# Kernel optimization log

Measured on AMD Instinct MI355X. Metric: run time of the kernel, lower is better.

## Reference

```python
import jax, jax.numpy as jnp
import numpy as np

BN_EPS = 1e-5


def conv(x, w, b=None, stride=1, pad=1):
    out = jax.lax.conv_general_dilated(
        x, w, (stride, stride), [(pad, pad), (pad, pad)],
        dimension_numbers=("NCHW", "OIHW", "NCHW"))
    if b is not None:
        out = out + b[None, :, None, None]
    return out


def bn_relu(x):
    # BatchNorm2d(affine=False) in training mode: per-channel batch stats
    mean = jnp.mean(x, axis=(0, 2, 3), keepdims=True)
    var = jnp.var(x, axis=(0, 2, 3), keepdims=True)
    return jax.nn.relu((x - mean) * jax.lax.rsqrt(var + BN_EPS))


def deform_conv(x, offset, w, b, stride, pad=1):
    # torchvision DeformConv2d semantics, 3x3 kernel, dilation=1
    B, C, H, W = x.shape
    O = w.shape[0]
    K = 9
    Ho, Wo = offset.shape[2], offset.shape[3]
    off = offset.reshape(B, K, 2, Ho, Wo)  # (dy, dx) per kernel tap
    ky, kx = jnp.meshgrid(jnp.arange(3), jnp.arange(3), indexing="ij")
    ky = ky.reshape(K).astype(x.dtype)
    kx = kx.reshape(K).astype(x.dtype)
    oy = (jnp.arange(Ho) * stride - pad).astype(x.dtype)
    ox = (jnp.arange(Wo) * stride - pad).astype(x.dtype)
    # sampling coords [B,K,Ho,Wo]
    ys = oy[None, None, :, None] + ky[None, :, None, None] + off[:, :, 0]
    xs = ox[None, None, None, :] + kx[None, :, None, None] + off[:, :, 1]
    y0 = jnp.floor(ys)
    x0 = jnp.floor(xs)
    wy1 = ys - y0
    wx1 = xs - x0
    imf = x.reshape(B, C, H * W)

    def gather(iy, ix):
        valid = (iy >= 0) & (iy <= H - 1) & (ix >= 0) & (ix <= W - 1)
        iyc = jnp.clip(iy, 0, H - 1).astype(jnp.int32)
        ixc = jnp.clip(ix, 0, W - 1).astype(jnp.int32)
        lin = iyc * W + ixc  # [B,K,Ho,Wo]
        g = jax.vmap(lambda im, li: im[:, li])(imf, lin)  # [B,C,K,Ho,Wo]
        return g * valid[:, None].astype(x.dtype)

    sampled = (gather(y0, x0) * ((1 - wy1) * (1 - wx1))[:, None]
               + gather(y0, x0 + 1) * ((1 - wy1) * wx1)[:, None]
               + gather(y0 + 1, x0) * (wy1 * (1 - wx1))[:, None]
               + gather(y0 + 1, x0 + 1) * (wy1 * wx1)[:, None])
    out = jnp.einsum("ock,bckhw->bohw", w.reshape(O, C, K), sampled)
    return out + b[None, :, None, None]


def avgpool4(x):
    B, C, H, W = x.shape
    return x.reshape(B, C, H // 4, 4, W // 4, 4).mean(axis=(3, 5))


def setup_inputs() -> dict:
    key = jax.random.key(0)
    ks = jax.random.split(key, 20)
    n = jax.random.normal
    s = 0.05
    return {
        "x": n(ks[0], (8, 3, 640, 640), jnp.float32),
        "w_off1": n(ks[1], (18, 3, 3, 3), jnp.float32) * s,
        "b_off1": jnp.zeros((18,), jnp.float32),
        "w_d1": n(ks[2], (64, 3, 3, 3), jnp.float32) * s,
        "b_d1": jnp.zeros((64,), jnp.float32),
        "w_skip": n(ks[3], (64, 3, 1, 1), jnp.float32) * s,
        "b_skip": jnp.zeros((64,), jnp.float32),
        "w_bl1": n(ks[4], (64, 64, 3, 3), jnp.float32) * s,
        "w_bl2": n(ks[5], (64, 64, 3, 3), jnp.float32) * s,
        "w_off2": n(ks[6], (18, 64, 3, 3), jnp.float32) * s,
        "b_off2": jnp.zeros((18,), jnp.float32),
        "w_d2": n(ks[7], (64, 64, 3, 3), jnp.float32) * s,
        "b_d2": jnp.zeros((64,), jnp.float32),
        "w_off3": n(ks[8], (18, 64, 3, 3), jnp.float32) * s,
        "b_off3": jnp.zeros((18,), jnp.float32),
        "w_d3": n(ks[9], (256, 64, 3, 3), jnp.float32) * s,
        "b_d3": jnp.zeros((256,), jnp.float32),
    }


def reference(x, w_off1, b_off1, w_d1, b_d1, w_skip, b_skip, w_bl1, w_bl2,
              w_off2, b_off2, w_d2, b_d2, w_off3, b_off3, w_d3, b_d3):
    offset1 = conv(x, w_off1, b_off1, stride=4)
    d1 = deform_conv(x, offset1, w_d1, b_d1, stride=4)
    skip = conv(avgpool4(x), w_skip, b_skip, stride=1, pad=0)
    f = bn_relu(conv(d1 + skip, w_bl1))
    feat_1_4 = bn_relu(conv(f, w_bl2))
    offset2 = conv(feat_1_4, w_off2, b_off2, stride=2)
    feat_1_8 = deform_conv(feat_1_4, offset2, w_d2, b_d2, stride=2)
    offset3 = conv(feat_1_8, w_off3, b_off3, stride=2)
    feat_1_16 = deform_conv(feat_1_8, offset3, w_d3, b_d3, stride=2)
    return (feat_1_4, feat_1_8, feat_1_16)
```

## Files before the change

kernel.cpp:

```cpp
#include <hip/hip_runtime.h>
#include <hip/hip_bf16.h>
#include <math.h>

#define TPB 256

typedef __attribute__((ext_vector_type(8))) short bf16x8_t;
typedef __attribute__((ext_vector_type(4))) float f32x4_t;
typedef __attribute__((ext_vector_type(4))) int i32x4_t;
typedef __attribute__((ext_vector_type(4))) unsigned short u16x4_t;

static __device__ __forceinline__ float bf16_to_f(unsigned short s) {
    union { unsigned u; float f; } cv;
    cv.u = ((unsigned)s) << 16;
    return cv.f;
}
static __device__ __forceinline__ short f_to_bf16(float v) {
    __hip_bfloat16 h = __float2bfloat16(v);
    return *(short*)&h;
}

__global__ void repack_frag_kernel(const float* __restrict__ w,
                                   short* __restrict__ wtf,
                                   int Oreal, int NFRAG)
{
    int idx = blockIdx.x * TPB + threadIdx.x;
    int total = 18 * NFRAG * 64 * 8;
    if (idx >= total) return;
    int j    = idx & 7;
    int lane = (idx >> 3) & 63;
    int t    = idx >> 9;
    int ocf  = t % NFRAG;
    int kc   = t / NFRAG;
    int oc   = ocf * 16 + (lane & 15);
    int tap  = kc >> 1;
    int ic   = (kc & 1) * 32 + (lane >> 4) * 8 + j;
    float v = 0.f;
    if (oc < Oreal)
        v = w[((size_t)(oc * 64 + ic)) * 9 + tap];
    wtf[idx] = f_to_bf16(v);
}

__global__ __launch_bounds__(256, 1) void conv3x3_mfma_kernel(
    const short* __restrict__ xh,
    const short* __restrict__ wt,
    short* __restrict__ outh,
    float* __restrict__ stats)
{
    __shared__ short tile[18 * 18 * 64];
    __shared__ float sstat[128];
    const int H = 160, W = 160, HW = 25600;
    int blk = blockIdx.x;
    int b  = blk / 100;
    int r  = blk % 100;
    int y0 = (r / 10) * 16;
    int x0 = (r % 10) * 16;
    const int tid = threadIdx.x;

    const short* inb = xh + (size_t)b * HW * 64;
    for (int item = tid; item < 18 * 18 * 8; item += TPB) {
        int c8  = item & 7;
        int pix = item >> 3;
        int col = pix % 18, row = pix / 18;
        int y = y0 + row - 1;
        int x = x0 + col - 1;
        bf16x8_t v = {};
        if (y >= 0 && y < H && x >= 0 && x < W)
            v = *(const bf16x8_t*)&inb[((size_t)y * W + x) * 64 + c8 * 8];
        int ch = c8 ^ (col & 7);
        *(bf16x8_t*)&tile[(row * 18 + col) * 64 + ch * 8] = v;
    }
    if (tid < 128) sstat[tid] = 0.f;
    __syncthreads();

    const int wv  = tid >> 6;
    const int l   = tid & 63;
    const int l15 = l & 15;
    const int lg  = l >> 4;

    f32x4_t acc[4][4];
#pragma unroll
    for (int i = 0; i < 4; ++i)
#pragma unroll
        for (int j = 0; j < 4; ++j)
            acc[i][j] = (f32x4_t){0.f, 0.f, 0.f, 0.f};

    bf16x8_t bfp[2][4], afp[2][4];
#pragma unroll
    for (int nf = 0; nf < 4; ++nf)
        bfp[0][nf] = *(const bf16x8_t*)(wt + (((size_t)(0 * 4 + nf)) * 64 + l) * 8);
    {
        int colr = l15;
        int chunk = lg ^ (colr & 7);
#pragma unroll
        for (int mf = 0; mf < 4; ++mf)
            afp[0][mf] = *(const bf16x8_t*)&tile[((wv * 4 + mf) * 18 + colr) * 64 + chunk * 8];
    }
#pragma unroll
    for (int kc = 0; kc < 18; ++kc) {
        const int cur = kc & 1, nxt = cur ^ 1;
        if (kc + 1 < 18) {
            int kn = kc + 1;
#pragma unroll
            for (int nf = 0; nf < 4; ++nf)
                bfp[nxt][nf] = *(const bf16x8_t*)(wt + (((size_t)(kn * 4 + nf)) * 64 + l) * 8);
            int tap = kn >> 1;
            int dy = tap / 3, dx = tap % 3;
            int colr = l15 + dx;
            int chunk = (((kn & 1) << 2) + lg) ^ (colr & 7);
#pragma unroll
            for (int mf = 0; mf < 4; ++mf)
                afp[nxt][mf] = *(const bf16x8_t*)&tile[((wv * 4 + mf + dy) * 18 + colr) * 64 + chunk * 8];
        }
#pragma unroll
        for (int mf = 0; mf < 4; ++mf)
#pragma unroll
            for (int nf = 0; nf < 4; ++nf)
                acc[mf][nf] = __builtin_amdgcn_mfma_f32_16x16x32_bf16(
                    afp[cur][mf], bfp[cur][nf], acc[mf][nf], 0, 0, 0);
    }

    short* outb = outh + (size_t)b * HW * 64;
#pragma unroll
    for (int mf = 0; mf < 4; ++mf) {
        int y = y0 + wv * 4 + mf;
#pragma unroll
        for (int nf = 0; nf < 4; ++nf) {
            int oc = nf * 16 + l15;
#pragma unroll
            for (int k = 0; k < 4; ++k)
                outb[((size_t)y * W + x0 + lg * 4 + k) * 64 + oc] = f_to_bf16(acc[mf][nf][k]);
        }
    }

#pragma unroll
    for (int nf = 0; nf < 4; ++nf) {
        float s = 0.f, s2 = 0.f;
#pragma unroll
        for (int mf = 0; mf < 4; ++mf)
#pragma unroll
            for (int k = 0; k < 4; ++k) {
                float v = acc[mf][nf][k];
                s += v; s2 += v * v;
            }
        s  += __shfl_xor(s, 16, 64);  s  += __shfl_xor(s, 32, 64);
        s2 += __shfl_xor(s2, 16, 64); s2 += __shfl_xor(s2, 32, 64);
        if (lg == 0) {
            int oc = nf * 16 + l15;
            atomicAdd(&sstat[oc], s);
            atomicAdd(&sstat[64 + oc], s2);
        }
    }
    __syncthreads();
    float* st = stats + (size_t)(blockIdx.x & 7) * 128;
    if (tid < 128) atomicAdd(&st[tid], sstat[tid]);
}

__global__ void nchw_to_nhwc_bf16_kernel(const float* __restrict__ in,
                                         short* __restrict__ out, int HW)
{
    __shared__ short tile[64][66];
    int nchunks = HW >> 6;
    int b  = blockIdx.x / nchunks;
    int p0 = (blockIdx.x % nchunks) << 6;
    int tid = threadIdx.x;
#pragma unroll
    for (int rep = 0; rep < 16; ++rep) {
        int item = rep * 256 + tid;
        int c = item >> 6, p = item & 63;
        tile[p][c] = f_to_bf16(in[((size_t)b * 64 + c) * HW + p0 + p]);
    }
    __syncthreads();
#pragma unroll
    for (int rep = 0; rep < 16; ++rep) {
        int item = rep * 256 + tid;
        int p = item >> 6, c = item & 63;
        out[((size_t)b * HW + p0 + p) * 64 + c] = tile[p][c];
    }
}

__global__ void bn_apply_elem_kernel(const short* __restrict__ in,
                                     const float* __restrict__ stats,
                                     short* __restrict__ outh,
                                     float invN)
{
    __shared__ float sm[64], sr[64];
    int tid = threadIdx.x;
    if (tid < 64) {
        float s = 0.f, s2 = 0.f;
#pragma unroll
        for (int k = 0; k < 8; ++k) {
            s  += stats[k * 128 + tid];
            s2 += stats[k * 128 + 64 + tid];
        }
        float mean = s * invN;
        float var  = s2 * invN - mean * mean;
        sm[tid] = mean;
        sr[tid] = rsqrtf(var + 1e-5f);
    }
    __syncthreads();
    int item = blockIdx.x * TPB + tid;
    int c0 = (item & 7) * 8;
    bf16x8_t v = *(const bf16x8_t*)&in[(size_t)item * 8];
    bf16x8_t o;
#pragma unroll
    for (int j = 0; j < 8; ++j) {
        float f = (bf16_to_f((unsigned short)v[j]) - sm[c0 + j]) * sr[c0 + j];
        o[j] = f_to_bf16(f > 0.f ? f : 0.f);
    }
    *(bf16x8_t*)&outh[(size_t)item * 8] = o;
}

__global__ void bn_apply_dual_kernel(const short* __restrict__ in,
                                     const float* __restrict__ stats,
                                     float* __restrict__ out,
                                     short* __restrict__ outh,
                                     int HW, float invN)
{
    __shared__ float ftile[64][65];
    __shared__ float sm[64], sr[64];
    int nchunks = HW >> 6;
    int b  = blockIdx.x / nchunks;
    int p0 = (blockIdx.x % nchunks) << 6;
    int tid = threadIdx.x;
    if (tid < 64) {
        float s = 0.f, s2 = 0.f;
#pragma unroll
        for (int k = 0; k < 8; ++k) {
            s  += stats[k * 128 + tid];
            s2 += stats[k * 128 + 64 + tid];
        }
        float mean = s * invN;
        float var  = s2 * invN - mean * mean;
        sm[tid] = mean;
        sr[tid] = rsqrtf(var + 1e-5f);
    }
    __syncthreads();
#pragma unroll
    for (int it = 0; it < 2; ++it) {
        int item = it * 256 + tid;
        int p = item >> 3, c0 = (item & 7) * 8;
        size_t gi = ((size_t)(b * HW + p0 + p)) * 64 + c0;
        bf16x8_t v = *(const bf16x8_t*)&in[gi];
        bf16x8_t o;
#pragma unroll
        for (int j = 0; j < 8; ++j) {
            float f = (bf16_to_f((unsigned short)v[j]) - sm[c0 + j]) * sr[c0 + j];
            f = f > 0.f ? f : 0.f;
            ftile[p][c0 + j] = f;
            o[j] = f_to_bf16(f);
        }
        *(bf16x8_t*)&outh[gi] = o;
    }
    __syncthreads();
#pragma unroll
    for (int rep = 0; rep < 16; ++rep) {
        int item = rep * 256 + tid;
        int c = item >> 6, p = item & 63;
        out[((size_t)b * 64 + c) * HW + p0 + p] = ftile[p][c];
    }
}

__global__ void x_to_nhwc4_kernel(const float* __restrict__ in,
                                  float* __restrict__ out)
{
    int idx = blockIdx.x * TPB + threadIdx.x;
    const int HW = 640 * 640;
    if (idx >= 8 * HW) return;
    int b = idx / HW, p = idx % HW;
    f32x4_t v;
    v[0] = in[((size_t)b * 3 + 0) * HW + p];
    v[1] = in[((size_t)b * 3 + 1) * HW + p];
    v[2] = in[((size_t)b * 3 + 2) * HW + p];
    v[3] = 0.f;
    *(f32x4_t*)&out[(size_t)idx * 4] = v;
}

__global__ void offset1_kernel(const float* __restrict__ x4,
                               const float* __restrict__ w,
                               const float* __restrict__ bias,
                               float* __restrict__ out)
{
    const int H = 640, W = 640, HW = 25600;
    int idx = blockIdx.x * TPB + threadIdx.x;
    if (idx >= 8 * HW) return;
    int b = idx / HW, r = idx % HW;
    int ho = r / 160, wo = r % 160;

    float acc[18];
#pragma unroll
    for (int o = 0; o < 18; ++o) acc[o] = bias[o];

    const float* xb = x4 + (size_t)b * H * W * 4;
#pragma unroll
    for (int tap = 0; tap < 9; ++tap) {
        int iy = ho * 4 - 1 + tap / 3;
        int ix = wo * 4 - 1 + tap % 3;
        if (iy < 0 || iy >= H || ix < 0 || ix >= W) continue;
        f32x4_t s = *(const f32x4_t*)&xb[((size_t)iy * W + ix) * 4];
#pragma unroll
        for (int c = 0; c < 3; ++c)
#pragma unroll
            for (int o = 0; o < 18; ++o)
                acc[o] += s[c] * w[(o * 3 + c) * 9 + tap];
    }
#pragma unroll
    for (int o = 0; o < 18; ++o)
        out[((size_t)(b * 18 + o)) * HW + r] = acc[o];
}

__global__ __launch_bounds__(256, 1) void offconv_mfma_kernel(
    const short* __restrict__ xh,
    const short* __restrict__ wt,
    const float* __restrict__ bias,
    float* __restrict__ out,
    int H, int W, int Ho, int Wo)
{
    const int HW = Ho * Wo;
    const int tid = threadIdx.x;
    const int wv = tid >> 6, l = tid & 63;
    const int l15 = l & 15, lg = l >> 4;
    const int pix0 = blockIdx.x * 64 + wv * 16;
    const int b = pix0 / HW;
    const int r0 = pix0 - b * HW;

    int rp = r0 + l15;
    int ho = rp / Wo, wo = rp % Wo;
    const short* xb = xh + (size_t)b * H * W * 64;

    f32x4_t acc[2];
    acc[0] = (f32x4_t){0.f, 0.f, 0.f, 0.f};
    acc[1] = (f32x4_t){0.f, 0.f, 0.f, 0.f};

#pragma unroll 2
    for (int kc = 0; kc < 18; ++kc) {
        int tap = kc >> 1;
        int iy = ho * 2 - 1 + tap / 3;
        int ix = wo * 2 - 1 + tap % 3;
        bf16x8_t af = {};
        if (iy >= 0 && iy < H && ix >= 0 && ix < W)
            af = *(const bf16x8_t*)&xb[((size_t)iy * W + ix) * 64
                                       + (kc & 1) * 32 + lg * 8];
#pragma unroll
        for (int nf = 0; nf < 2; ++nf) {
            bf16x8_t bf = *(const bf16x8_t*)(wt + (((size_t)(kc * 2 + nf)) * 64 + l) * 8);
            acc[nf] = __builtin_amdgcn_mfma_f32_16x16x32_bf16(af, bf, acc[nf], 0, 0, 0);
        }
    }

#pragma unroll
    for (int nf = 0; nf < 2; ++nf) {
        int oc = nf * 16 + l15;
        if (oc < 18) {
            float bv = bias[oc];
            f32x4_t v = acc[nf];
            v[0] += bv; v[1] += bv; v[2] += bv; v[3] += bv;
            *(f32x4_t*)&out[((size_t)(b * 18 + oc)) * HW + r0 + lg * 4] = v;
        }
    }
}

__global__ __launch_bounds__(256, 1) void deform1_kernel(
    const float* __restrict__ x4,
    const float* __restrict__ off,
    const float* __restrict__ w,
    const float* __restrict__ bias,
    const float* __restrict__ pool,
    const float* __restrict__ wsk,
    const float* __restrict__ bsk,
    short* __restrict__ outh)
{
    const int H = 640, W = 640, Ho = 160, Wo = 160, HW = 25600;
    constexpr int P = 32;
    __shared__ float samp[P][28];
    __shared__ int   sidx[P * 9][4];
    __shared__ float swt[P * 9][4];
    const int tid = threadIdx.x;
    const int pix0 = blockIdx.x * P;
    const int b = pix0 / HW;
    const int r0 = pix0 - b * HW;

    for (int item = tid; item < P * 9; item += TPB) {
        int p = item / 9, tap = item % 9;
        int r = r0 + p, ho = r / Wo, wo = r % Wo;
        float dy = off[((size_t)(b * 18 + 2 * tap) * Ho + ho) * Wo + wo];
        float dx = off[((size_t)(b * 18 + 2 * tap + 1) * Ho + ho) * Wo + wo];
        float ys = (float)(ho * 4 - 1 + tap / 3) + dy;
        float xs = (float)(wo * 4 - 1 + tap % 3) + dx;
        float y0f = floorf(ys), x0f = floorf(xs);
        float fy = ys - y0f, fx = xs - x0f;
        int y0 = (int)y0f, x0 = (int)x0f;
        float wts[4] = {(1.f - fy) * (1.f - fx), (1.f - fy) * fx,
                        fy * (1.f - fx),          fy * fx};
#pragma unroll
        for (int j = 0; j < 4; ++j) {
            int iy = y0 + (j >> 1), ix = x0 + (j & 1);
            bool v = (iy >= 0) && (iy < H) && (ix >= 0) && (ix < W);
            sidx[item][j] = v ? (iy * W + ix) : 0;
            swt[item][j]  = v ? wts[j] : 0.f;
        }
    }
    __syncthreads();

    const float* xb = x4 + (size_t)b * H * W * 4;
    for (int item = tid; item < P * 9; item += TPB) {
        int p = item / 9, tap = item % 9;
        i32x4_t id4 = *(const i32x4_t*)sidx[item];
        f32x4_t w4  = *(const f32x4_t*)swt[item];
        f32x4_t a0 = *(const f32x4_t*)&xb[(size_t)(unsigned)id4[0] * 4];
        f32x4_t a1 = *(const f32x4_t*)&xb[(size_t)(unsigned)id4[1] * 4];
        f32x4_t a2 = *(const f32x4_t*)&xb[(size_t)(unsigned)id4[2] * 4];
        f32x4_t a3 = *(const f32x4_t*)&xb[(size_t)(unsigned)id4[3] * 4];
        samp[p][0 * 9 + tap] = w4[0]*a0[0] + w4[1]*a1[0] + w4[2]*a2[0] + w4[3]*a3[0];
        samp[p][1 * 9 + tap] = w4[0]*a0[1] + w4[1]*a1[1] + w4[2]*a2[1] + w4[3]*a3[1];
        samp[p][2 * 9 + tap] = w4[0]*a0[2] + w4[1]*a1[2] + w4[2]*a2[2] + w4[3]*a3[2];
    }
    __syncthreads();

    int g = tid >> 6;
    int o = tid & 63;
    float acc[8];
#pragma unroll
    for (int pi = 0; pi < 8; ++pi) acc[pi] = bias[o] + bsk[o];
#pragma unroll
    for (int c = 0; c < 3; ++c)
#pragma unroll
        for (int k = 0; k < 9; ++k) {
            float wv = w[((size_t)(o * 3 + c)) * 9 + k];
#pragma unroll
            for (int pi = 0; pi < 8; ++pi)
                acc[pi] += wv * samp[g * 8 + pi][c * 9 + k];
        }
#pragma unroll
    for (int pi = 0; pi < 8; ++pi) {
        int r = r0 + g * 8 + pi;
        float sv = wsk[o * 3 + 0] * pool[(size_t)(b * 3 + 0) * HW + r]
                 + wsk[o * 3 + 1] * pool[(size_t)(b * 3 + 1) * HW + r]
                 + wsk[o * 3 + 2] * pool[(size_t)(b * 3 + 2) * HW + r];
        outh[((size_t)(b * HW + r)) * 64 + o] = f_to_bf16(acc[pi] + sv);
    }
}

template <int O>
__global__ __launch_bounds__(256, 1) void deform_mfma_kernel(
    const short* __restrict__ xh,
    const float* __restrict__ off,
    const short* __restrict__ wt,
    const float* __restrict__ bias,
    float* __restrict__ out,
    int H, int W, int Ho, int Wo, int stride)
{
    constexpr int NF = O / 64;
    constexpr int NFRAG = O / 16;
    constexpr int P  = 32;
    __shared__ alignas(16) short samp[P * 576];
    __shared__ int   sidx[P * 9][4];
    __shared__ float swt[P * 9][4];

    const int tid = threadIdx.x;
    const int HW = Ho * Wo;
    const int pix0 = blockIdx.x * P;
    const int b = pix0 / HW;
    const int r0 = pix0 - b * HW;

    for (int item = tid; item < P * 9; item += TPB) {
        int p = item / 9, tap = item % 9;
        int r = r0 + p, ho = r / Wo, wo = r % Wo;
        float dy = off[((size_t)(b * 18 + 2 * tap) * Ho + ho) * Wo + wo];
        float dx = off[((size_t)(b * 18 + 2 * tap + 1) * Ho + ho) * Wo + wo];
        float ys = (float)(ho * stride - 1 + tap / 3) + dy;
        float xs = (float)(wo * stride - 1 + tap % 3) + dx;
        float y0f = floorf(ys), x0f = floorf(xs);
        float fy = ys - y0f, fx = xs - x0f;
        int y0 = (int)y0f, x0 = (int)x0f;
        float wts[4] = {(1.f - fy) * (1.f - fx), (1.f - fy) * fx,
                        fy * (1.f - fx),          fy * fx};
#pragma unroll
        for (int j = 0; j < 4; ++j) {
            int iy = y0 + (j >> 1), ix = x0 + (j & 1);
            bool v = (iy >= 0) && (iy < H) && (ix >= 0) && (ix < W);
            sidx[item][j] = v ? (iy * W + ix) : 0;
            swt[item][j]  = v ? wts[j] : 0.f;
        }
    }
    __syncthreads();

    {
        const int grp = tid >> 4;
        const int ic  = (tid & 15) * 4;
        const short* xb = xh + (size_t)b * H * W * 64;
#pragma unroll 3
        for (int i = 0; i < 18; ++i) {
            int e = grp * 18 + i;
            int p = e / 9, tap = e % 9;
            i32x4_t id4 = *(const i32x4_t*)sidx[e];
            f32x4_t w4  = *(const f32x4_t*)swt[e];
            u16x4_t u0 = *(const u16x4_t*)&xb[(size_t)(unsigned)id4[0] * 64 + ic];
            u16x4_t u1 = *(const u16x4_t*)&xb[(size_t)(unsigned)id4[1] * 64 + ic];
            u16x4_t u2 = *(const u16x4_t*)&xb[(size_t)(unsigned)id4[2] * 64 + ic];
            u16x4_t u3 = *(const u16x4_t*)&xb[(size_t)(unsigned)id4[3] * 64 + ic];
            float v0 = w4[0]*bf16_to_f(u0[0]) + w4[1]*bf16_to_f(u1[0])
                     + w4[2]*bf16_to_f(u2[0]) + w4[3]*bf16_to_f(u3[0]);
            float v1 = w4[0]*bf16_to_f(u0[1]) + w4[1]*bf16_to_f(u1[1])
                     + w4[2]*bf16_to_f(u2[1]) + w4[3]*bf16_to_f(u3[1]);
            float v2 = w4[0]*bf16_to_f(u0[2]) + w4[1]*bf16_to_f(u1[2])
                     + w4[2]*bf16_to_f(u2[2]) + w4[3]*bf16_to_f(u3[2]);
            float v3 = w4[0]*bf16_to_f(u0[3]) + w4[1]*bf16_to_f(u1[3])
                     + w4[2]*bf16_to_f(u2[3]) + w4[3]*bf16_to_f(u3[3]);
            int sw = (tap * 8 + ((ic >> 3) ^ (p & 7))) * 8 + (ic & 7);
            short* dst = &samp[p * 576 + sw];
            dst[0] = f_to_bf16(v0);
            dst[1] = f_to_bf16(v1);
            dst[2] = f_to_bf16(v2);
            dst[3] = f_to_bf16(v3);
        }
    }
    __syncthreads();

    const int wv = tid >> 6;
    const int l  = tid & 63;
    const int l15 = l & 15, lg = l >> 4;
    f32x4_t acc[2][NF];
#pragma unroll
    for (int mf = 0; mf < 2; ++mf)
#pragma unroll
        for (int nf = 0; nf < NF; ++nf)
            acc[mf][nf] = (f32x4_t){0.f, 0.f, 0.f, 0.f};

#pragma unroll 2
    for (int kc = 0; kc < 18; ++kc) {
        int tap = kc >> 1;
        int low = (((kc & 1) << 2) | lg) ^ (l15 & 7);
        bf16x8_t af0 = *(const bf16x8_t*)&samp[l15 * 576 + (tap * 8 + low) * 8];
        bf16x8_t af1 = *(const bf16x8_t*)&samp[(l15 + 16) * 576 + (tap * 8 + low) * 8];
#pragma unroll
        for (int nf = 0; nf < NF; ++nf) {
            int ocf = wv * NF + nf;
            bf16x8_t bf = *(const bf16x8_t*)(wt + (((size_t)(kc * NFRAG + ocf)) * 64 + l) * 8);
            acc[0][nf] = __builtin_amdgcn_mfma_f32_16x16x32_bf16(af0, bf, acc[0][nf], 0, 0, 0);
            acc[1][nf] = __builtin_amdgcn_mfma_f32_16x16x32_bf16(af1, bf, acc[1][nf], 0, 0, 0);
        }
    }

#pragma unroll
    for (int mf = 0; mf < 2; ++mf)
#pragma unroll
        for (int nf = 0; nf < NF; ++nf) {
            int oc = (wv * NF + nf) * 16 + l15;
            float bv = bias[oc];
            f32x4_t v = acc[mf][nf];
            v[0] += bv; v[1] += bv; v[2] += bv; v[3] += bv;
            *(f32x4_t*)&out[((size_t)(b * O + oc)) * HW + r0 + mf * 16 + lg * 4] = v;
        }
}

__global__ void avgpool4_kernel(const float* __restrict__ in,
                                float* __restrict__ out,
                                int BC, int Ho, int Wo, int H, int W)
{
    int idx = blockIdx.x * TPB + threadIdx.x;
    int total = BC * Ho * Wo;
    if (idx >= total) return;
    int wo = idx % Wo;
    int t = idx / Wo;
    int ho = t % Ho;
    int bc = t / Ho;
    const float* xp = in + (size_t)bc * H * W + (ho * 4) * W + wo * 4;
    float s = 0.f;
#pragma unroll
    for (int i = 0; i < 4; ++i)
#pragma unroll
        for (int j = 0; j < 4; ++j)
            s += xp[i * W + j];
    out[idx] = s * (1.0f / 16.0f);
}

__global__ void zero_stats_kernel(float* __restrict__ stats)
{
    int i = threadIdx.x;
#pragma unroll
    for (int k = 0; k < 8; ++k) stats[k * 256 + i] = 0.f;
}

extern "C" void kernel_launch(void* const* d_in, const int* in_sizes, int n_in,
                              void* d_out, int out_size, void* d_ws, size_t ws_size,
                              hipStream_t stream)
{
    const float* x      = (const float*)d_in[0];
    const float* w_off1 = (const float*)d_in[1];
    const float* b_off1 = (const float*)d_in[2];
    const float* w_d1   = (const float*)d_in[3];
    const float* b_d1   = (const float*)d_in[4];
    const float* w_skip = (const float*)d_in[5];
    const float* b_skip = (const float*)d_in[6];
    const float* w_bl1  = (const float*)d_in[7];
    const float* w_bl2  = (const float*)d_in[8];
    const float* w_off2 = (const float*)d_in[9];
    const float* b_off2 = (const float*)d_in[10];
    const float* w_d2   = (const float*)d_in[11];
    const float* b_d2   = (const float*)d_in[12];
    const float* w_off3 = (const float*)d_in[13];
    const float* b_off3 = (const float*)d_in[14];
    const float* w_d3   = (const float*)d_in[15];
    const float* b_d3   = (const float*)d_in[16];

    const int B = 8;
    float* A     = (float*)d_ws;
    float* bufB  = A + 3686400;
    float* bufC  = bufB + 13107200;

    short* hB   = (short*)bufB;
    short* hC   = (short*)bufC;
    float* pool = bufB + 8000000;

    short* wt1    = (short*)(A + 1000000);
    short* wt2    = wt1 + 18 * 4 * 512;
    short* wtd2   = (short*)(A + 1500000);
    short* wtd3   = (short*)(A + 1550000);
    short* wtoff2 = (short*)(A + 1700000);
    short* wtoff3 = (short*)(A + 1712000);
    float* stats1 = A + 1800000;
    float* stats2 = stats1 + 1024;

    float* out0 = (float*)d_out;
    float* out1 = out0 + 13107200;
    float* out2 = out1 + 3276800;

    const float invN = 1.0f / (B * 25600);

    x_to_nhwc4_kernel<<<(8 * 409600 + TPB - 1) / TPB, TPB, 0, stream>>>(x, bufC);

    offset1_kernel<<<(8 * 25600 + TPB - 1) / TPB, TPB, 0, stream>>>(
        bufC, w_off1, b_off1, A);

    avgpool4_kernel<<<(B * 3 * 25600 + TPB - 1) / TPB, TPB, 0, stream>>>(
        x, pool, B * 3, 160, 160, 640, 640);

    deform1_kernel<<<8 * 25600 / 32, TPB, 0, stream>>>(
        bufC, A, w_d1, b_d1, pool, w_skip, b_skip, hB);

    repack_frag_kernel<<<(18 * 4 * 512 + TPB - 1) / TPB, TPB, 0, stream>>>(w_bl1, wt1, 64, 4);
    repack_frag_kernel<<<(18 * 4 * 512 + TPB - 1) / TPB, TPB, 0, stream>>>(w_bl2, wt2, 64, 4);
    repack_frag_kernel<<<(18 * 4 * 512 + TPB - 1) / TPB, TPB, 0, stream>>>(w_d2, wtd2, 64, 4);
    repack_frag_kernel<<<(18 * 16 * 512 + TPB - 1) / TPB, TPB, 0, stream>>>(w_d3, wtd3, 256, 16);
    repack_frag_kernel<<<(18 * 2 * 512 + TPB - 1) / TPB, TPB, 0, stream>>>(w_off2, wtoff2, 18, 2);
    repack_frag_kernel<<<(18 * 2 * 512 + TPB - 1) / TPB, TPB, 0, stream>>>(w_off3, wtoff3, 18, 2);
    zero_stats_kernel<<<1, 256, 0, stream>>>(stats1);

    conv3x3_mfma_kernel<<<800, TPB, 0, stream>>>(hB, wt1, hC, stats1);

    bn_apply_elem_kernel<<<8 * 25600 * 8 / TPB, TPB, 0, stream>>>(
        hC, stats1, hB, invN);

    conv3x3_mfma_kernel<<<800, TPB, 0, stream>>>(hB, wt2, hC, stats2);

    bn_apply_dual_kernel<<<8 * 400, TPB, 0, stream>>>(
        hC, stats2, out0, hB, 25600, invN);

    offconv_mfma_kernel<<<8 * 6400 / 64, TPB, 0, stream>>>(
        hB, wtoff2, b_off2, A, 160, 160, 80, 80);

    deform_mfma_kernel<64><<<8 * 6400 / 32, TPB, 0, stream>>>(
        hB, A, wtd2, b_d2, out1, 160, 160, 80, 80, 2);

    nchw_to_nhwc_bf16_kernel<<<8 * (6400 / 64), TPB, 0, stream>>>(out1, hC, 6400);

    offconv_mfma_kernel<<<8 * 1600 / 64, TPB, 0, stream>>>(
        hC, wtoff3, b_off3, A, 80, 80, 40, 40);

    deform_mfma_kernel<256><<<8 * 1600 / 32, TPB, 0, stream>>>(
        hC, A, wtd3, b_d3, out2, 80, 80, 40, 40, 2);
}
```

Before: 253.0 us.

## Stage conv3x3 output through LDS for coalesced stores and allow two blocks per CU

The 3x3 MFMA conv kernel now writes its accumulators into the shared tile and then stores 16-byte vectors per pixel, instead of scattered 2-byte global stores. The halo load becomes a fixed unrolled loop that reads from a zeroed page for out-of-bounds pixels, removing the branch. The swizzle moves from the LDS write address to the global read address. Launch bounds are raised to two blocks per CU for more occupancy, at the cost of register pressure and two extra barriers.

```diff
diff --git a/kernel.cpp b/kernel.cpp
--- a/kernel.cpp
+++ b/kernel.cpp
@@ -40,13 +40,14 @@
     wtf[idx] = f_to_bf16(v);
 }
 
-__global__ __launch_bounds__(256, 1) void conv3x3_mfma_kernel(
+__global__ __launch_bounds__(256, 2) void conv3x3_mfma_kernel(
     const short* __restrict__ xh,
     const short* __restrict__ wt,
     short* __restrict__ outh,
-    float* __restrict__ stats)
-{
-    __shared__ short tile[18 * 18 * 64];
+    float* __restrict__ stats,
+    const float* __restrict__ zp)
+{
+    __shared__ short tile[2816 * 8];
     __shared__ float sstat[128];
     const int H = 160, W = 160, HW = 25600;
     int blk = blockIdx.x;
@@ -55,19 +56,22 @@
     int y0 = (r / 10) * 16;
     int x0 = (r % 10) * 16;
     const int tid = threadIdx.x;
-
     const short* inb = xh + (size_t)b * HW * 64;
-    for (int item = tid; item < 18 * 18 * 8; item += TPB) {
+
+#pragma unroll
+    for (int it = 0; it < 11; ++it) {
+        int item = it * 256 + tid;
         int c8  = item & 7;
         int pix = item >> 3;
-        int col = pix % 18, row = pix / 18;
+        int row = pix / 18;
+        int col = pix - row * 18;
         int y = y0 + row - 1;
         int x = x0 + col - 1;
-        bf16x8_t v = {};
-        if (y >= 0 && y < H && x >= 0 && x < W)
-            v = *(const bf16x8_t*)&inb[((size_t)y * W + x) * 64 + c8 * 8];
-        int ch = c8 ^ (col & 7);
-        *(bf16x8_t*)&tile[(row * 18 + col) * 64 + ch * 8] = v;
+        bool ok = (pix < 324) & (y >= 0) & (y < H) & (x >= 0) & (x < W);
+        const short* src = ok
+            ? &inb[((size_t)y * W + x) * 64 + ((c8 ^ (col & 7)) << 3)]
+            : (const short*)zp;
+        *(bf16x8_t*)&tile[item * 8] = *(const bf16x8_t*)src;
     }
     if (tid < 128) sstat[tid] = 0.f;
     __syncthreads();
@@ -119,17 +123,28 @@
                     afp[cur][mf], bfp[cur][nf], acc[mf][nf], 0, 0, 0);
     }
 
-    short* outb = outh + (size_t)b * HW * 64;
+    __syncthreads();
 #pragma unroll
     for (int mf = 0; mf < 4; ++mf) {
-        int y = y0 + wv * 4 + mf;
+        int py = wv * 4 + mf;
 #pragma unroll
         for (int nf = 0; nf < 4; ++nf) {
             int oc = nf * 16 + l15;
 #pragma unroll
             for (int k = 0; k < 4; ++k)
-                outb[((size_t)y * W + x0 + lg * 4 + k) * 64 + oc] = f_to_bf16(acc[mf][nf][k]);
-        }
+                tile[((py * 16) + lg * 4 + k) * 64 + oc] = f_to_bf16(acc[mf][nf][k]);
+        }
+    }
+    __syncthreads();
+    short* outb = outh + (size_t)b * HW * 64;
+#pragma unroll
+    for (int j = 0; j < 8; ++j) {
+        int item = j * 256 + tid;
+        int c8  = item & 7;
+        int pix = item >> 3;
+        int py  = pix >> 4, px = pix & 15;
+        *(bf16x8_t*)&outb[((size_t)(y0 + py) * W + x0 + px) * 64 + c8 * 8] =
+            *(bf16x8_t*)&tile[pix * 64 + c8 * 8];
     }
 
 #pragma unroll
@@ -579,6 +594,8 @@
     int i = threadIdx.x;
 #pragma unroll
     for (int k = 0; k < 8; ++k) stats[k * 256 + i] = 0.f;
+    stats[2048 + i] = 0.f;
+    stats[2048 + 256 + i] = 0.f;
 }
 
 extern "C" void kernel_launch(void* const* d_in, const int* in_sizes, int n_in,
@@ -620,6 +637,7 @@
     short* wtoff3 = (short*)(A + 1712000);
     float* stats1 = A + 1800000;
     float* stats2 = stats1 + 1024;
+    float* zpage  = stats1 + 2048;
 
     float* out0 = (float*)d_out;
     float* out1 = out0 + 13107200;
@@ -646,12 +664,12 @@
     repack_frag_kernel<<<(18 * 2 * 512 + TPB - 1) / TPB, TPB, 0, stream>>>(w_off3, wtoff3, 18, 2);
     zero_stats_kernel<<<1, 256, 0, stream>>>(stats1);
 
-    conv3x3_mfma_kernel<<<800, TPB, 0, stream>>>(hB, wt1, hC, stats1);
+    conv3x3_mfma_kernel<<<800, TPB, 0, stream>>>(hB, wt1, hC, stats1, zpage);
 
     bn_apply_elem_kernel<<<8 * 25600 * 8 / TPB, TPB, 0, stream>>>(
         hC, stats1, hB, invN);
 
-    conv3x3_mfma_kernel<<<800, TPB, 0, stream>>>(hB, wt2, hC, stats2);
+    conv3x3_mfma_kernel<<<800, TPB, 0, stream>>>(hB, wt2, hC, stats2, zpage);
 
     bn_apply_dual_kernel<<<8 * 400, TPB, 0, stream>>>(
         hC, stats2, out0, hB, 25600, invN);
```

Result: no change. 251.8 us (-0.4%).
